# Kernel tuning notes

Measured on AMD Instinct MI355X. Metric: run time of the kernel, lower is better.

## Reference

```python
import jax, jax.numpy as jnp
import numpy as np

B, T, D = 2, 2048, 1024
H = 16
HD = D // H


def setup_inputs() -> dict:
    key = jax.random.key(0)
    ks = jax.random.split(key, 9)
    s = 1.0 / np.sqrt(D)
    return {
        "x": jax.random.normal(ks[0], (B, T, D), dtype=jnp.float32),
        "Wq": jax.random.normal(ks[1], (D, D), dtype=jnp.float32) * s,
        "bq": jax.random.normal(ks[2], (D,), dtype=jnp.float32) * s,
        "Wk": jax.random.normal(ks[3], (D, D), dtype=jnp.float32) * s,
        "bk": jax.random.normal(ks[4], (D,), dtype=jnp.float32) * s,
        "Wv": jax.random.normal(ks[5], (D, D), dtype=jnp.float32) * s,
        "bv": jax.random.normal(ks[6], (D,), dtype=jnp.float32) * s,
        "Wo": jax.random.normal(ks[7], (D, D), dtype=jnp.float32) * s,
        "bo": jax.random.normal(ks[8], (D,), dtype=jnp.float32) * s,
    }


def reference(x, Wq, bq, Wk, bk, Wv, bv, Wo, bo):
    b, t, d = x.shape
    # projections; torch Linear computes x @ W.T + b
    def proj(W, bias):
        y = jnp.einsum("btd,ed->bte", x, W) + bias
        return y.reshape(b, t, H, HD).transpose(0, 2, 1, 3)  # [B,H,T,HD]
    q = proj(Wq, bq)
    k = proj(Wk, bk)
    v = proj(Wv, bv)
    scores = jnp.einsum("bhqd,bhkd->bhqk", q, k) / np.sqrt(HD)  # [B,H,T,T]
    causal = jnp.triu(jnp.ones((t, t), dtype=bool), k=1)
    scores = jnp.where(causal[None, None], jnp.float32(-1e9), scores)
    attn = jax.nn.softmax(scores, axis=-1)
    out = jnp.einsum("bhqk,bhkd->bhqd", attn, v)  # [B,H,T,HD]
    out = out.transpose(0, 2, 1, 3).reshape(b, t, d)
    return jnp.einsum("btd,ed->bte", out, Wo) + bo
```

## Files before the change

kernel.cpp:

```cpp
#include <hip/hip_runtime.h>


#define DEV __device__ __forceinline__

typedef __attribute__((ext_vector_type(8))) __bf16 bf16x8;
typedef __attribute__((ext_vector_type(4))) float f32x4;

DEV unsigned short f2bf(float f) {
  union { float f; unsigned u; } c;
  c.f = f;
  unsigned u = c.u + 0x7FFFu + ((c.u >> 16) & 1u);
  return (unsigned short)(u >> 16);
}

DEV unsigned cvtpk(float lo, float hi) {
  unsigned r;
  asm("v_cvt_pk_bf16_f32 %0, %1, %2" : "=v"(r) : "v"(lo), "v"(hi));
  return r;
}

DEV void gload16(const unsigned short* g, unsigned short* l) {
  __builtin_amdgcn_global_load_lds(
      (const __attribute__((address_space(1))) unsigned int*)g,
      (__attribute__((address_space(3))) unsigned int*)l, 16, 0, 0);
}

DEV f32x4 mfma16(bf16x8 a, bf16x8 b, f32x4 c) {
  return __builtin_amdgcn_mfma_f32_16x16x32_bf16(a, b, c, 0, 0, 0);
}

#define WAITVM(n) asm volatile("s_waitcnt vmcnt(" #n ")" ::: "memory")
#define WAITLGKM() asm volatile("s_waitcnt lgkmcnt(0)" ::: "memory")
#define BAR() __builtin_amdgcn_s_barrier()
#define SCHEDB() __builtin_amdgcn_sched_barrier(0)

__global__ __launch_bounds__(256) void k_cvt_all(
    const float* __restrict__ x, const float* __restrict__ wq,
    const float* __restrict__ wk, const float* __restrict__ wv,
    const float* __restrict__ wo, unsigned short* __restrict__ dst) {
  int i = blockIdx.x * blockDim.x + threadIdx.x;
  const float* s;
  int off;
  if (i < 1048576) {
    s = x; off = i;
  } else {
    int j = i - 1048576;
    int w = j >> 18;
    off = j & 262143;
    s = (w == 0) ? wq : (w == 1) ? wk : (w == 2) ? wv : wo;
  }
  float4 v = reinterpret_cast<const float4*>(s)[off];
  uint2 o;
  o.x = (unsigned)f2bf(v.x) | ((unsigned)f2bf(v.y) << 16);
  o.y = (unsigned)f2bf(v.z) | ((unsigned)f2bf(v.w) << 16);
  reinterpret_cast<uint2*>(dst)[i] = o;
}

DEV void gemm_stage(const unsigned short* __restrict__ A,
                    const unsigned short* __restrict__ W,
                    unsigned short* la, unsigned short* lb,
                    int m0, int n0, int k0, int tid) {
#pragma unroll
  for (int i = 0; i < 2; ++i) {
    const int c = i * 256 + tid;
    const int row = c >> 2;
    const int scb = (((c & 3) << 4)) ^ ((row & 3) << 4);
    gload16(A + (m0 + row) * 1024 + k0 + (scb >> 1),
            (unsigned short*)((char*)la + c * 16));
    gload16(W + (n0 + row) * 1024 + k0 + (scb >> 1),
            (unsigned short*)((char*)lb + c * 16));
  }
}

DEV void gemm_core_128(const unsigned short* __restrict__ A,
                       const unsigned short* __restrict__ W,
                       unsigned short* la0, unsigned short* lb0,
                       int m0, int n0, f32x4 (&acc)[4][4]) {
  const int tid = threadIdx.x;
  const int lane = tid & 63;
  const int wave = tid >> 6;
  const int wm = (wave >> 1) * 64, wn = (wave & 1) * 64;
  const int g16 = ((lane >> 4) << 4);
  const int sx = (lane & 3) << 4;

  gemm_stage(A, W, la0, lb0, m0, n0, 0, tid);
  __syncthreads();

  for (int kt = 0; kt < 32; ++kt) {
    const int cur = kt & 1;
    unsigned short* la = la0 + cur * 4096;
    unsigned short* lb = lb0 + cur * 4096;
    if (kt + 1 < 32)
      gemm_stage(A, W, la0 + (cur ^ 1) * 4096, lb0 + (cur ^ 1) * 4096, m0, n0,
                 (kt + 1) * 32, tid);
    bf16x8 af[4], bfr[4];
#pragma unroll
    for (int m = 0; m < 4; ++m)
      af[m] = *reinterpret_cast<const bf16x8*>(
          (char*)la + (wm + m * 16 + (lane & 15)) * 64 + (g16 ^ sx));
#pragma unroll
    for (int n = 0; n < 4; ++n)
      bfr[n] = *reinterpret_cast<const bf16x8*>(
          (char*)lb + (wn + n * 16 + (lane & 15)) * 64 + (g16 ^ sx));
#pragma unroll
    for (int m = 0; m < 4; ++m)
#pragma unroll
      for (int n = 0; n < 4; ++n)
        acc[m][n] = mfma16(af[m], bfr[n], acc[m][n]);
    __syncthreads();
  }
}

__global__ __launch_bounds__(256) void k_gemm_qkv(
    const unsigned short* __restrict__ X, const unsigned short* __restrict__ Wq,
    const unsigned short* __restrict__ Wk, const unsigned short* __restrict__ Wv,
    const float* __restrict__ bq, const float* __restrict__ bk,
    const float* __restrict__ bv, unsigned short* __restrict__ Qo,
    unsigned short* __restrict__ Ko, unsigned short* __restrict__ Vo) {
  __shared__ unsigned short ls[16384];
  const int mode = blockIdx.z;
  const unsigned short* W = (mode == 0) ? Wq : (mode == 1) ? Wk : Wv;
  const float* bias = (mode == 0) ? bq : (mode == 1) ? bk : bv;
  const int m0 = blockIdx.y * 128, n0 = blockIdx.x * 128;
  f32x4 acc[4][4] = {};
  gemm_core_128(X, W, ls, ls + 8192, m0, n0, acc);

  const int lane = threadIdx.x & 63, wave = threadIdx.x >> 6;
  const int l15 = lane & 15, g = lane >> 4;
  const int wm = (wave >> 1) * 64, wn = (wave & 1) * 64;
  unsigned short* lw = ls + wave * 4096;

  const int h = (n0 + wn) >> 6;
  const int rbase0 = m0 + wm;
  const int b = rbase0 >> 11;
  const int tb0 = rbase0 & 2047;

  if (mode == 2) {
#pragma unroll
    for (int m = 0; m < 4; ++m)
#pragma unroll
      for (int n = 0; n < 4; ++n) {
        const float bb = bias[n0 + wn + n * 16 + l15];
        uint2 w;
        w.x = cvtpk(acc[m][n][0] + bb, acc[m][n][1] + bb);
        w.y = cvtpk(acc[m][n][2] + bb, acc[m][n][3] + bb);
        *reinterpret_cast<uint2*>(
            (char*)lw + (n * 16 + l15) * 128 +
            ((((m << 2) + g) ^ (l15 & 14)) << 3)) = w;
      }
    WAITLGKM();
    SCHEDB();
#pragma unroll
    for (int it = 0; it < 8; ++it) {
      const int hd = (lane >> 3) + it * 8;
      const int jj = ((lane & 7) << 1) ^ (hd & 14);
      uint4 v = *reinterpret_cast<const uint4*>((char*)lw + hd * 128 + jj * 8);
      *reinterpret_cast<uint4*>(
          &Vo[((((b << 4) + h) << 6) + hd) * 2048 + tb0 + ((lane & 7) << 3)]) =
          v;
    }
  } else {
    const float sc = (mode == 0) ? 0.180336880f : 1.0f;
#pragma unroll
    for (int m = 0; m < 4; ++m)
#pragma unroll
      for (int n = 0; n < 4; ++n) {
        const float bb = bias[n0 + wn + n * 16 + l15];
#pragma unroll
        for (int r = 0; r < 4; ++r)
          lw[(m * 16 + (g << 2) + r) * 64 + n * 16 + l15] =
              f2bf((acc[m][n][r] + bb) * sc);
      }
    WAITLGKM();
    SCHEDB();
    unsigned short* dst = (mode == 0) ? Qo : Ko;
#pragma unroll
    for (int it = 0; it < 8; ++it) {
      const int rr = (lane >> 3) + it * 8;
      const int ck = (lane & 7) * 8;
      uint4 v = *reinterpret_cast<const uint4*>(&lw[rr * 64 + ck]);
      *reinterpret_cast<uint4*>(
          &dst[(((b << 4) + h) * 2048 + tb0 + rr) * 64 + ck]) = v;
    }
  }
}

__global__ __launch_bounds__(256) void k_gemm_out(
    const unsigned short* __restrict__ Ctx, const unsigned short* __restrict__ Wo,
    const float* __restrict__ bo, float* __restrict__ Out) {
  __shared__ unsigned short ls[16384];
  unsigned short* la0 = ls;
  unsigned short* lb0 = ls + 8192;
  const int tid = threadIdx.x;
  const int lane = tid & 63, wave = tid >> 6;
  const int l15 = lane & 15, g = lane >> 4;
  const int m0 = blockIdx.y * 128, n0 = blockIdx.x * 64;
  const int wm = (wave >> 1) * 64, wn = (wave & 1) * 32;
  const int g16 = (g << 4);
  const int sx = (lane & 3) << 4;
  f32x4 acc[4][2] = {};

#define STG_OUT(buf, k0)                                                     \
  {                                                                          \
    _Pragma("unroll") for (int i = 0; i < 2; ++i) {                          \
      const int c = i * 256 + tid;                                           \
      const int row = c >> 2;                                                \
      const int scb = (((c & 3) << 4)) ^ ((row & 3) << 4);                   \
      gload16(Ctx + (m0 + row) * 1024 + (k0) + (scb >> 1),                   \
              (unsigned short*)((char*)(la0 + (buf)*4096) + c * 16));        \
    }                                                                        \
    {                                                                        \
      const int row = tid >> 2;                                              \
      const int scb = (((tid & 3) << 4)) ^ ((row & 3) << 4);                 \
      gload16(Wo + (n0 + row) * 1024 + (k0) + (scb >> 1),                    \
              (unsigned short*)((char*)(lb0 + (buf)*2048) + tid * 16));      \
    }                                                                        \
  }

  STG_OUT(0, 0);
  __syncthreads();

  for (int kt = 0; kt < 32; ++kt) {
    const int cur = kt & 1;
    unsigned short* la = la0 + cur * 4096;
    unsigned short* lb = lb0 + cur * 2048;
    if (kt + 1 < 32) STG_OUT(cur ^ 1, (kt + 1) * 32);
    bf16x8 af[4], bfr[2];
#pragma unroll
    for (int m = 0; m < 4; ++m)
      af[m] = *reinterpret_cast<const bf16x8*>(
          (char*)la + (wm + m * 16 + l15) * 64 + (g16 ^ sx));
#pragma unroll
    for (int n = 0; n < 2; ++n)
      bfr[n] = *reinterpret_cast<const bf16x8*>(
          (char*)lb + (wn + n * 16 + l15) * 64 + (g16 ^ sx));
#pragma unroll
    for (int m = 0; m < 4; ++m)
#pragma unroll
      for (int n = 0; n < 2; ++n)
        acc[m][n] = mfma16(af[m], bfr[n], acc[m][n]);
    __syncthreads();
  }
#undef STG_OUT

  float* lwf = (float*)(ls + wave * 4096);
#pragma unroll
  for (int m = 0; m < 4; ++m)
#pragma unroll
    for (int n = 0; n < 2; ++n) {
      const float bb = bo[n0 + wn + n * 16 + l15];
#pragma unroll
      for (int r = 0; r < 4; ++r)
        lwf[(m * 16 + (g << 2) + r) * 32 + n * 16 + l15] = acc[m][n][r] + bb;
    }
  WAITLGKM();
  SCHEDB();
#pragma unroll
  for (int it = 0; it < 8; ++it) {
    const int rr = (lane >> 3) + it * 8;
    const int ck = (lane & 7) * 4;
    float4 v = *reinterpret_cast<const float4*>(&lwf[rr * 32 + ck]);
    *reinterpret_cast<float4*>(&Out[(m0 + wm + rr) * 1024 + n0 + wn + ck]) = v;
  }
}


DEV void attn_stage(const unsigned short* __restrict__ Kb,
                    const unsigned short* __restrict__ Vb,
                    unsigned short* lk, unsigned short* lv, int kv0, int tid) {
#pragma unroll
  for (int i = 0; i < 2; ++i) {
    const int c = i * 256 + tid;
    const int row = c >> 3;
    const int cb = (c & 7) << 4;
    const int scb = cb ^ ((row & 7) << 4);
    gload16(Kb + (kv0 + row) * 64 + (scb >> 1),
            (unsigned short*)((char*)lk + c * 16));
    gload16(Vb + row * 2048 + kv0 + (scb >> 1),
            (unsigned short*)((char*)lv + c * 16));
  }
}

DEV void attn_step(const unsigned short* lk, const unsigned short* lv,
                   unsigned short (&lp)[16][72], const bf16x8 (&qf)[2],
                   f32x4 (&o)[4], float& lsum, int lane, int qloc, bool diag) {
  const int g = lane >> 4;
  f32x4 st[4];
#pragma unroll
  for (int n = 0; n < 4; ++n) {
    f32x4 z = {};
    const int row = n * 16 + (lane & 15);
    const int sw = (row & 7) << 4;
#pragma unroll
    for (int kk = 0; kk < 2; ++kk) {
      bf16x8 kf = *reinterpret_cast<const bf16x8*>(
          (char*)lk + row * 128 + ((kk * 64 + (g << 4)) ^ sw));
      z = mfma16(kf, qf[kk], z);
    }
    st[n] = z;
  }
  if (diag) {
#pragma unroll
    for (int n = 0; n < 4; ++n)
#pragma unroll
      for (int r = 0; r < 4; ++r)
        if (n * 16 + g * 4 + r > qloc) st[n][r] = -1e30f;
  }
  float rs = 0.f;
#pragma unroll
  for (int n = 0; n < 4; ++n)
#pragma unroll
    for (int r = 0; r < 4; ++r) {
      float p = exp2f(st[n][r]);
      st[n][r] = p;
      rs += p;
    }
  lsum += rs;
#pragma unroll
  for (int n = 0; n < 4; ++n) {
    uint2 w;
    w.x = cvtpk(st[n][0], st[n][1]);
    w.y = cvtpk(st[n][2], st[n][3]);
    *reinterpret_cast<uint2*>(&lp[lane & 15][n * 16 + g * 4]) = w;
  }
  WAITLGKM();
  SCHEDB();
  bf16x8 pb[2];
  pb[0] = *reinterpret_cast<const bf16x8*>(&lp[lane & 15][g * 8]);
  pb[1] = *reinterpret_cast<const bf16x8*>(&lp[lane & 15][32 + g * 8]);
#pragma unroll
  for (int h = 0; h < 4; ++h) {
    const int row = h * 16 + (lane & 15);
    const int sw = (row & 7) << 4;
#pragma unroll
    for (int kk = 0; kk < 2; ++kk) {
      bf16x8 vf = *reinterpret_cast<const bf16x8*>(
          (char*)lv + row * 128 + ((kk * 64 + (g << 4)) ^ sw));
      o[h] = mfma16(vf, pb[kk], o[h]);
    }
  }
}

DEV void attn_step_dual(const unsigned short* lk, const unsigned short* lv,
                        unsigned short (&lpA)[16][72],
                        unsigned short (&lpB)[16][72],
                        const bf16x8 (&qfA)[2], const bf16x8 (&qfB)[2],
                        f32x4 (&oA)[4], f32x4 (&oB)[4], float& lsA, float& lsB,
                        int lane, int qloc, bool diagA) {
  const int g = lane >> 4;
  f32x4 sA[4], sB[4];
#pragma unroll
  for (int n = 0; n < 4; ++n) {
    f32x4 zA = {}, zB = {};
    const int row = n * 16 + (lane & 15);
    const int sw = (row & 7) << 4;
#pragma unroll
    for (int kk = 0; kk < 2; ++kk) {
      bf16x8 kf = *reinterpret_cast<const bf16x8*>(
          (char*)lk + row * 128 + ((kk * 64 + (g << 4)) ^ sw));
      zB = mfma16(kf, qfB[kk], zB);
      zA = mfma16(kf, qfA[kk], zA);
    }
    sA[n] = zA;
    sB[n] = zB;
  }
  if (diagA) {
#pragma unroll
    for (int n = 0; n < 4; ++n)
#pragma unroll
      for (int r = 0; r < 4; ++r)
        if (n * 16 + g * 4 + r > qloc) sA[n][r] = -1e30f;
  }
  float rsA = 0.f, rsB = 0.f;
#pragma unroll
  for (int n = 0; n < 4; ++n)
#pragma unroll
    for (int r = 0; r < 4; ++r) {
      float pA = exp2f(sA[n][r]);
      float pB = exp2f(sB[n][r]);
      sA[n][r] = pA;
      sB[n][r] = pB;
      rsA += pA;
      rsB += pB;
    }
  lsA += rsA;
  lsB += rsB;
#pragma unroll
  for (int n = 0; n < 4; ++n) {
    uint2 wA, wB;
    wA.x = cvtpk(sA[n][0], sA[n][1]);
    wA.y = cvtpk(sA[n][2], sA[n][3]);
    wB.x = cvtpk(sB[n][0], sB[n][1]);
    wB.y = cvtpk(sB[n][2], sB[n][3]);
    *reinterpret_cast<uint2*>(&lpA[lane & 15][n * 16 + g * 4]) = wA;
    *reinterpret_cast<uint2*>(&lpB[lane & 15][n * 16 + g * 4]) = wB;
  }
  WAITLGKM();
  SCHEDB();
  bf16x8 pbA[2], pbB[2];
  pbA[0] = *reinterpret_cast<const bf16x8*>(&lpA[lane & 15][g * 8]);
  pbA[1] = *reinterpret_cast<const bf16x8*>(&lpA[lane & 15][32 + g * 8]);
  pbB[0] = *reinterpret_cast<const bf16x8*>(&lpB[lane & 15][g * 8]);
  pbB[1] = *reinterpret_cast<const bf16x8*>(&lpB[lane & 15][32 + g * 8]);
#pragma unroll
  for (int h = 0; h < 4; ++h) {
    const int row = h * 16 + (lane & 15);
    const int sw = (row & 7) << 4;
#pragma unroll
    for (int kk = 0; kk < 2; ++kk) {
      bf16x8 vf = *reinterpret_cast<const bf16x8*>(
          (char*)lv + row * 128 + ((kk * 64 + (g << 4)) ^ sw));
      oB[h] = mfma16(vf, pbB[kk], oB[h]);
      oA[h] = mfma16(vf, pbA[kk], oA[h]);
    }
  }
}

DEV void attn_epi(unsigned short* __restrict__ Ctx,
                  unsigned short (&lp)[16][72], const f32x4 (&o)[4],
                  float lsum, int b, int hh, int qbase, int lane) {
  float lt = lsum;
  lt += __shfl_xor(lt, 16);
  lt += __shfl_xor(lt, 32);
  const float inv = 1.f / lt;
  const int g = lane >> 4;
#pragma unroll
  for (int h = 0; h < 4; ++h) {
    uint2 w;
    w.x = cvtpk(o[h][0] * inv, o[h][1] * inv);
    w.y = cvtpk(o[h][2] * inv, o[h][3] * inv);
    *reinterpret_cast<uint2*>(&lp[lane & 15][h * 16 + g * 4]) = w;
  }
  WAITLGKM();
  SCHEDB();
#pragma unroll
  for (int it = 0; it < 2; ++it) {
    const int q = (lane >> 3) + it * 8;
    const int ck = (lane & 7) * 8;
    uint4 v = *reinterpret_cast<const uint4*>(&lp[q][ck]);
    *reinterpret_cast<uint4*>(
        &Ctx[(b * 2048 + qbase + q) * 1024 + hh * 64 + ck]) = v;
  }
}

__global__ __launch_bounds__(256) void k_attn(
    const unsigned short* __restrict__ Q, const unsigned short* __restrict__ K,
    const unsigned short* __restrict__ Vt, unsigned short* __restrict__ Ctx) {
  __shared__ unsigned short lk[3][64 * 64];
  __shared__ unsigned short lv[3][64 * 64];
  __shared__ unsigned short lp[8][16][72];

  const int tid = threadIdx.x, lane = tid & 63, wave = tid >> 6;
  const int ip = blockIdx.x, bh = blockIdx.y;
  const int qtA = ip;
  const int qtB = 31 - ip;
  const int nt = qtB + 1;

  const unsigned short* Kb = K + bh * 2048 * 64;
  const unsigned short* Vb = Vt + bh * 64 * 2048;

  bf16x8 qfA[2], qfB[2];
  {
    const unsigned short* qr =
        Q + (bh * 2048 + qtA * 64 + wave * 16 + (lane & 15)) * 64 + ((lane >> 4) << 3);
    qfA[0] = *reinterpret_cast<const bf16x8*>(qr);
    qfA[1] = *reinterpret_cast<const bf16x8*>(qr + 32);
    qr = Q + (bh * 2048 + qtB * 64 + wave * 16 + (lane & 15)) * 64 + ((lane >> 4) << 3);
    qfB[0] = *reinterpret_cast<const bf16x8*>(qr);
    qfB[1] = *reinterpret_cast<const bf16x8*>(qr + 32);
  }

  f32x4 oA[4] = {}, oB[4] = {};
  float lA = 0.f, lB = 0.f;
  const int qloc = wave * 16 + (lane & 15);

  attn_stage(Kb, Vb, lk[0], lv[0], 0, tid);
  attn_stage(Kb, Vb, lk[1], lv[1], 64, tid);
  WAITVM(4);
  BAR();

  for (int t = 0; t < nt; ++t) {
    const int nx = (t + 2 < nt) ? t + 2 : nt - 1;
    const int sb = (t + 2) % 3, cb = t % 3;
    attn_stage(Kb, Vb, lk[sb], lv[sb], nx * 64, tid);
    WAITVM(8);
    BAR();
    SCHEDB();
    if (t <= qtA)
      attn_step_dual(lk[cb], lv[cb], lp[wave], lp[wave + 4], qfA, qfB, oA,
                     oB, lA, lB, lane, qloc, t == qtA);
    else
      attn_step(lk[cb], lv[cb], lp[wave + 4], qfB, oB, lB, lane, qloc,
                t == qtB);
    BAR();
  }

  const int b = bh >> 4, hh = bh & 15;
  attn_epi(Ctx, lp[wave], oA, lA, b, hh, qtA * 64 + wave * 16, lane);
  attn_epi(Ctx, lp[wave + 4], oB, lB, b, hh, qtB * 64 + wave * 16, lane);
}

extern "C" void kernel_launch(void* const* d_in, const int* in_sizes, int n_in,
                              void* d_out, int out_size, void* d_ws,
                              size_t ws_size, hipStream_t stream) {
  const float* x = (const float*)d_in[0];
  const float* Wq = (const float*)d_in[1];
  const float* bq = (const float*)d_in[2];
  const float* Wk = (const float*)d_in[3];
  const float* bk = (const float*)d_in[4];
  const float* Wv = (const float*)d_in[5];
  const float* bv = (const float*)d_in[6];
  const float* Wo = (const float*)d_in[7];
  const float* bo = (const float*)d_in[8];
  float* out = (float*)d_out;

  char* ws = (char*)d_ws;
  unsigned short* xb = (unsigned short*)(ws);
  unsigned short* wqb = (unsigned short*)(ws + (8u << 20));
  unsigned short* wkb = (unsigned short*)(ws + (10u << 20));
  unsigned short* wvb = (unsigned short*)(ws + (12u << 20));
  unsigned short* wob = (unsigned short*)(ws + (14u << 20));
  unsigned short* Qb = (unsigned short*)(ws + (16u << 20));
  unsigned short* Kb = (unsigned short*)(ws + (24u << 20));
  unsigned short* Vtb = (unsigned short*)(ws + (32u << 20));
  unsigned short* Ctx = (unsigned short*)(ws + (40u << 20));

  k_cvt_all<<<8192, 256, 0, stream>>>(x, Wq, Wk, Wv, Wo, xb);

  k_gemm_qkv<<<dim3(8, 32, 3), 256, 0, stream>>>(xb, wqb, wkb, wvb, bq, bk, bv,
                                                 Qb, Kb, Vtb);
  k_attn<<<dim3(16, 32), 256, 0, stream>>>(Qb, Kb, Vtb, Ctx);
  k_gemm_out<<<dim3(16, 32), 256, 0, stream>>>(Ctx, wob, bo, out);
}
```

Measured before the change: 124.6 us.

## Software-pipeline attention loop: overlap QK of tile t with softmax/PV of t-1

Splits the per-tile attention step into a QK score phase and a softmax plus PV phase. The loop now computes the scores for tile t while finishing the exponentials and PV products for tile t-1, so MFMA work and dependent ALU work from neighbouring tiles can interleave. The V staging ring grows from 3 to 4 buffers so the previous tile's V stays valid. The loop also drops from two barriers per iteration to one. In exchange it holds more registers for the carried score tiles and uses more LDS, which may reduce occupancy.

```diff
diff --git a/kernel.cpp b/kernel.cpp
--- a/kernel.cpp
+++ b/kernel.cpp
@@ -281,11 +281,9 @@
   }
 }
 
-DEV void attn_step(const unsigned short* lk, const unsigned short* lv,
-                   unsigned short (&lp)[16][72], const bf16x8 (&qf)[2],
-                   f32x4 (&o)[4], float& lsum, int lane, int qloc, bool diag) {
+DEV void qk1(const unsigned short* lk, const bf16x8 (&qf)[2], f32x4 (&st)[4],
+             int lane, int qloc, bool diag) {
   const int g = lane >> 4;
-  f32x4 st[4];
 #pragma unroll
   for (int n = 0; n < 4; ++n) {
     f32x4 z = {};
@@ -306,21 +304,54 @@
       for (int r = 0; r < 4; ++r)
         if (n * 16 + g * 4 + r > qloc) st[n][r] = -1e30f;
   }
+}
+
+DEV void qk_dual(const unsigned short* lk, const bf16x8 (&qfA)[2],
+                 const bf16x8 (&qfB)[2], f32x4 (&sA)[4], f32x4 (&sB)[4],
+                 int lane, int qloc, bool diagA) {
+  const int g = lane >> 4;
+#pragma unroll
+  for (int n = 0; n < 4; ++n) {
+    f32x4 zA = {}, zB = {};
+    const int row = n * 16 + (lane & 15);
+    const int sw = (row & 7) << 4;
+#pragma unroll
+    for (int kk = 0; kk < 2; ++kk) {
+      bf16x8 kf = *reinterpret_cast<const bf16x8*>(
+          (char*)lk + row * 128 + ((kk * 64 + (g << 4)) ^ sw));
+      zB = mfma16(kf, qfB[kk], zB);
+      zA = mfma16(kf, qfA[kk], zA);
+    }
+    sA[n] = zA;
+    sB[n] = zB;
+  }
+  if (diagA) {
+#pragma unroll
+    for (int n = 0; n < 4; ++n)
+#pragma unroll
+      for (int r = 0; r < 4; ++r)
+        if (n * 16 + g * 4 + r > qloc) sA[n][r] = -1e30f;
+  }
+}
+
+DEV void finish1(const unsigned short* lv, unsigned short (&lp)[16][72],
+                 f32x4 (&p)[4], f32x4 (&o)[4], float& lsum, int lane) {
+  const int g = lane >> 4;
   float rs = 0.f;
 #pragma unroll
   for (int n = 0; n < 4; ++n)
 #pragma unroll
     for (int r = 0; r < 4; ++r) {
-      float p = exp2f(st[n][r]);
-      st[n][r] = p;
-      rs += p;
+      float v = exp2f(p[n][r]);
+      p[n][r] = v;
+      rs += v;
     }
   lsum += rs;
 #pragma unroll
   for (int n = 0; n < 4; ++n) {
     uint2 w;
-    w.x = cvtpk(st[n][0], st[n][1]);
-    w.y = cvtpk(st[n][2], st[n][3]);
+    w.x = cvtpk(p[n][0], p[n][1]);
+    w.y = cvtpk(p[n][2], p[n][3]);
     *reinterpret_cast<uint2*>(&lp[lane & 15][n * 16 + g * 4]) = w;
   }
   WAITLGKM();
@@ -341,57 +372,32 @@
   }
 }
 
-DEV void attn_step_dual(const unsigned short* lk, const unsigned short* lv,
-                        unsigned short (&lpA)[16][72],
-                        unsigned short (&lpB)[16][72],
-                        const bf16x8 (&qfA)[2], const bf16x8 (&qfB)[2],
-                        f32x4 (&oA)[4], f32x4 (&oB)[4], float& lsA, float& lsB,
-                        int lane, int qloc, bool diagA) {
+DEV void finish_dual(const unsigned short* lv, unsigned short (&lpA)[16][72],
+                     unsigned short (&lpB)[16][72], f32x4 (&pA)[4],
+                     f32x4 (&pB)[4], f32x4 (&oA)[4], f32x4 (&oB)[4],
+                     float& lsA, float& lsB, int lane) {
   const int g = lane >> 4;
-  f32x4 sA[4], sB[4];
-#pragma unroll
-  for (int n = 0; n < 4; ++n) {
-    f32x4 zA = {}, zB = {};
-    const int row = n * 16 + (lane & 15);
-    const int sw = (row & 7) << 4;
-#pragma unroll
-    for (int kk = 0; kk < 2; ++kk) {
-      bf16x8 kf = *reinterpret_cast<const bf16x8*>(
-          (char*)lk + row * 128 + ((kk * 64 + (g << 4)) ^ sw));
-      zB = mfma16(kf, qfB[kk], zB);
-      zA = mfma16(kf, qfA[kk], zA);
-    }
-    sA[n] = zA;
-    sB[n] = zB;
-  }
-  if (diagA) {
-#pragma unroll
-    for (int n = 0; n < 4; ++n)
-#pragma unroll
-      for (int r = 0; r < 4; ++r)
-        if (n * 16 + g * 4 + r > qloc) sA[n][r] = -1e30f;
-  }
   float rsA = 0.f, rsB = 0.f;
 #pragma unroll
   for (int n = 0; n < 4; ++n)
 #pragma unroll
     for (int r = 0; r < 4; ++r) {
-      float pA = exp2f(sA[n][r]);
-      float pB = exp2f(sB[n][r]);
-      sA[n][r] = pA;
-      sB[n][r] = pB;
-      rsA += pA;
-      rsB += pB;
+      float vA = exp2f(pA[n][r]);
+      float vB = exp2f(pB[n][r]);
+      pA[n][r] = vA;
+      pB[n][r] = vB;
+      rsA += vA;
+      rsB += vB;
     }
   lsA += rsA;
   lsB += rsB;
 #pragma unroll
   for (int n = 0; n < 4; ++n) {
     uint2 wA, wB;
-    wA.x = cvtpk(sA[n][0], sA[n][1]);
-    wA.y = cvtpk(sA[n][2], sA[n][3]);
-    wB.x = cvtpk(sB[n][0], sB[n][1]);
-    wB.y = cvtpk(sB[n][2], sB[n][3]);
+    wA.x = cvtpk(pA[n][0], pA[n][1]);
+    wA.y = cvtpk(pA[n][2], pA[n][3]);
+    wB.x = cvtpk(pB[n][0], pB[n][1]);
+    wB.y = cvtpk(pB[n][2], pB[n][3]);
     *reinterpret_cast<uint2*>(&lpA[lane & 15][n * 16 + g * 4]) = wA;
     *reinterpret_cast<uint2*>(&lpB[lane & 15][n * 16 + g * 4]) = wB;
   }
@@ -446,8 +452,8 @@
 __global__ __launch_bounds__(256) void k_attn(
     const unsigned short* __restrict__ Q, const unsigned short* __restrict__ K,
     const unsigned short* __restrict__ Vt, unsigned short* __restrict__ Ctx) {
-  __shared__ unsigned short lk[3][64 * 64];
-  __shared__ unsigned short lv[3][64 * 64];
+  __shared__ unsigned short lk[3 * 4096];
+  __shared__ unsigned short lv[4 * 4096];
   __shared__ unsigned short lp[8][16][72];
 
   const int tid = threadIdx.x, lane = tid & 63, wave = tid >> 6;
@@ -471,29 +477,43 @@
   }
 
   f32x4 oA[4] = {}, oB[4] = {};
+  f32x4 pA[4], pB[4];
   float lA = 0.f, lB = 0.f;
   const int qloc = wave * 16 + (lane & 15);
 
-  attn_stage(Kb, Vb, lk[0], lv[0], 0, tid);
-  attn_stage(Kb, Vb, lk[1], lv[1], 64, tid);
-  WAITVM(4);
-  BAR();
+  attn_stage(Kb, Vb, lk, lv, 0, tid);
+  attn_stage(Kb, Vb, lk + 4096, lv + 4096, 64, tid);
 
   for (int t = 0; t < nt; ++t) {
-    const int nx = (t + 2 < nt) ? t + 2 : nt - 1;
-    const int sb = (t + 2) % 3, cb = t % 3;
-    attn_stage(Kb, Vb, lk[sb], lv[sb], nx * 64, tid);
-    WAITVM(8);
+    WAITVM(4);
     BAR();
-    SCHEDB();
-    if (t <= qtA)
-      attn_step_dual(lk[cb], lv[cb], lp[wave], lp[wave + 4], qfA, qfB, oA,
-                     oB, lA, lB, lane, qloc, t == qtA);
+    {
+      const int nx = (t + 2 < nt) ? t + 2 : nt - 1;
+      attn_stage(Kb, Vb, lk + ((t + 2) % 3) * 4096, lv + ((t + 2) & 3) * 4096,
+                 nx * 64, tid);
+    }
+    const unsigned short* lkc = lk + (t % 3) * 4096;
+    f32x4 sA[4], sB[4];
+    const bool dual = (t <= qtA);
+    if (dual)
+      qk_dual(lkc, qfA, qfB, sA, sB, lane, qloc, t == qtA);
     else
-      attn_step(lk[cb], lv[cb], lp[wave + 4], qfB, oB, lB, lane, qloc,
-                t == qtB);
-    BAR();
-  }
+      qk1(lkc, qfB, sB, lane, qloc, t == qtB);
+    if (t > 0) {
+      const unsigned short* lvp = lv + ((t - 1) & 3) * 4096;
+      if (t - 1 <= qtA)
+        finish_dual(lvp, lp[wave], lp[wave + 4], pA, pB, oA, oB, lA, lB, lane);
+      else
+        finish1(lvp, lp[wave + 4], pB, oB, lB, lane);
+    }
+#pragma unroll
+    for (int n = 0; n < 4; ++n) pB[n] = sB[n];
+    if (dual) {
+#pragma unroll
+      for (int n = 0; n < 4; ++n) pA[n] = sA[n];
+    }
+  }
+  finish1(lv + ((nt - 1) & 3) * 4096, lp[wave + 4], pB, oB, lB, lane);
 
   const int b = bh >> 4, hh = bh & 15;
   attn_epi(Ctx, lp[wave], oA, lA, b, hh, qtA * 64 + wave * 16, lane);
```

New measurement: 171.3 us. 37.5% more time.

## Split paired causal query tiles across 8 waves and add MFMA priority hints

Applied to the files above, without the earlier changes.

The attention kernel moves from 256 to 512 threads per block. Waves 0-3 process the late query tile B and waves 4-7 the early tile A, replacing the dual-tile step in which each wave handled both. Each thread now stages one 16-byte chunk of K and V per tile, and the vmcnt waits are adjusted to match. s_setprio raises wave priority around the MFMA sections. The goal is more wave-level parallelism and latency hiding with fewer registers per wave, but the A waves go idle at the barriers for the remainder of the loop.

```diff
diff --git a/kernel.cpp b/kernel.cpp
--- a/kernel.cpp
+++ b/kernel.cpp
@@ -33,6 +33,7 @@
 #define WAITLGKM() asm volatile("s_waitcnt lgkmcnt(0)" ::: "memory")
 #define BAR() __builtin_amdgcn_s_barrier()
 #define SCHEDB() __builtin_amdgcn_sched_barrier(0)
+#define PRIO(n) __builtin_amdgcn_s_setprio(n)
 
 __global__ __launch_bounds__(256) void k_cvt_all(
     const float* __restrict__ x, const float* __restrict__ wq,
@@ -268,17 +269,14 @@
 DEV void attn_stage(const unsigned short* __restrict__ Kb,
                     const unsigned short* __restrict__ Vb,
                     unsigned short* lk, unsigned short* lv, int kv0, int tid) {
-#pragma unroll
-  for (int i = 0; i < 2; ++i) {
-    const int c = i * 256 + tid;
-    const int row = c >> 3;
-    const int cb = (c & 7) << 4;
-    const int scb = cb ^ ((row & 7) << 4);
-    gload16(Kb + (kv0 + row) * 64 + (scb >> 1),
-            (unsigned short*)((char*)lk + c * 16));
-    gload16(Vb + row * 2048 + kv0 + (scb >> 1),
-            (unsigned short*)((char*)lv + c * 16));
-  }
+  const int c = tid;
+  const int row = c >> 3;
+  const int cb = (c & 7) << 4;
+  const int scb = cb ^ ((row & 7) << 4);
+  gload16(Kb + (kv0 + row) * 64 + (scb >> 1),
+          (unsigned short*)((char*)lk + c * 16));
+  gload16(Vb + row * 2048 + kv0 + (scb >> 1),
+          (unsigned short*)((char*)lv + c * 16));
 }
 
 DEV void attn_step(const unsigned short* lk, const unsigned short* lv,
@@ -286,6 +284,7 @@
                    f32x4 (&o)[4], float& lsum, int lane, int qloc, bool diag) {
   const int g = lane >> 4;
   f32x4 st[4];
+  PRIO(1);
 #pragma unroll
   for (int n = 0; n < 4; ++n) {
     f32x4 z = {};
@@ -299,6 +298,7 @@
     }
     st[n] = z;
   }
+  PRIO(0);
   if (diag) {
 #pragma unroll
     for (int n = 0; n < 4; ++n)
@@ -328,6 +328,7 @@
   bf16x8 pb[2];
   pb[0] = *reinterpret_cast<const bf16x8*>(&lp[lane & 15][g * 8]);
   pb[1] = *reinterpret_cast<const bf16x8*>(&lp[lane & 15][32 + g * 8]);
+  PRIO(1);
 #pragma unroll
   for (int h = 0; h < 4; ++h) {
     const int row = h * 16 + (lane & 15);
@@ -339,81 +340,7 @@
       o[h] = mfma16(vf, pb[kk], o[h]);
     }
   }
-}
-
-DEV void attn_step_dual(const unsigned short* lk, const unsigned short* lv,
-                        unsigned short (&lpA)[16][72],
-                        unsigned short (&lpB)[16][72],
-                        const bf16x8 (&qfA)[2], const bf16x8 (&qfB)[2],
-                        f32x4 (&oA)[4], f32x4 (&oB)[4], float& lsA, float& lsB,
-                        int lane, int qloc, bool diagA) {
-  const int g = lane >> 4;
-  f32x4 sA[4], sB[4];
-#pragma unroll
-  for (int n = 0; n < 4; ++n) {
-    f32x4 zA = {}, zB = {};
-    const int row = n * 16 + (lane & 15);
-    const int sw = (row & 7) << 4;
-#pragma unroll
-    for (int kk = 0; kk < 2; ++kk) {
-      bf16x8 kf = *reinterpret_cast<const bf16x8*>(
-          (char*)lk + row * 128 + ((kk * 64 + (g << 4)) ^ sw));
-      zB = mfma16(kf, qfB[kk], zB);
-      zA = mfma16(kf, qfA[kk], zA);
-    }
-    sA[n] = zA;
-    sB[n] = zB;
-  }
-  if (diagA) {
-#pragma unroll
-    for (int n = 0; n < 4; ++n)
-#pragma unroll
-      for (int r = 0; r < 4; ++r)
-        if (n * 16 + g * 4 + r > qloc) sA[n][r] = -1e30f;
-  }
-  float rsA = 0.f, rsB = 0.f;
-#pragma unroll
-  for (int n = 0; n < 4; ++n)
-#pragma unroll
-    for (int r = 0; r < 4; ++r) {
-      float pA = exp2f(sA[n][r]);
-      float pB = exp2f(sB[n][r]);
-      sA[n][r] = pA;
-      sB[n][r] = pB;
-      rsA += pA;
-      rsB += pB;
-    }
-  lsA += rsA;
-  lsB += rsB;
-#pragma unroll
-  for (int n = 0; n < 4; ++n) {
-    uint2 wA, wB;
-    wA.x = cvtpk(sA[n][0], sA[n][1]);
-    wA.y = cvtpk(sA[n][2], sA[n][3]);
-    wB.x = cvtpk(sB[n][0], sB[n][1]);
-    wB.y = cvtpk(sB[n][2], sB[n][3]);
-    *reinterpret_cast<uint2*>(&lpA[lane & 15][n * 16 + g * 4]) = wA;
-    *reinterpret_cast<uint2*>(&lpB[lane & 15][n * 16 + g * 4]) = wB;
-  }
-  WAITLGKM();
-  SCHEDB();
-  bf16x8 pbA[2], pbB[2];
-  pbA[0] = *reinterpret_cast<const bf16x8*>(&lpA[lane & 15][g * 8]);
-  pbA[1] = *reinterpret_cast<const bf16x8*>(&lpA[lane & 15][32 + g * 8]);
-  pbB[0] = *reinterpret_cast<const bf16x8*>(&lpB[lane & 15][g * 8]);
-  pbB[1] = *reinterpret_cast<const bf16x8*>(&lpB[lane & 15][32 + g * 8]);
-#pragma unroll
-  for (int h = 0; h < 4; ++h) {
-    const int row = h * 16 + (lane & 15);
-    const int sw = (row & 7) << 4;
-#pragma unroll
-    for (int kk = 0; kk < 2; ++kk) {
-      bf16x8 vf = *reinterpret_cast<const bf16x8*>(
-          (char*)lv + row * 128 + ((kk * 64 + (g << 4)) ^ sw));
-      oB[h] = mfma16(vf, pbB[kk], oB[h]);
-      oA[h] = mfma16(vf, pbA[kk], oA[h]);
-    }
-  }
+  PRIO(0);
 }
 
 DEV void attn_epi(unsigned short* __restrict__ Ctx,
@@ -443,11 +370,11 @@
   }
 }
 
-__global__ __launch_bounds__(256) void k_attn(
+__global__ __launch_bounds__(512) void k_attn(
     const unsigned short* __restrict__ Q, const unsigned short* __restrict__ K,
     const unsigned short* __restrict__ Vt, unsigned short* __restrict__ Ctx) {
-  __shared__ unsigned short lk[3][64 * 64];
-  __shared__ unsigned short lv[3][64 * 64];
+  __shared__ unsigned short lk[3 * 4096];
+  __shared__ unsigned short lv[3 * 4096];
   __shared__ unsigned short lp[8][16][72];
 
   const int tid = threadIdx.x, lane = tid & 63, wave = tid >> 6;
@@ -456,48 +383,47 @@
   const int qtB = 31 - ip;
   const int nt = qtB + 1;
 
+  const bool isB = wave < 4;
+  const int wv4 = wave & 3;
+  const int qt = isB ? qtB : qtA;
+  const int myNt = isB ? nt : qtA + 1;
+
   const unsigned short* Kb = K + bh * 2048 * 64;
   const unsigned short* Vb = Vt + bh * 64 * 2048;
 
-  bf16x8 qfA[2], qfB[2];
+  bf16x8 qf[2];
   {
     const unsigned short* qr =
-        Q + (bh * 2048 + qtA * 64 + wave * 16 + (lane & 15)) * 64 + ((lane >> 4) << 3);
-    qfA[0] = *reinterpret_cast<const bf16x8*>(qr);
-    qfA[1] = *reinterpret_cast<const bf16x8*>(qr + 32);
-    qr = Q + (bh * 2048 + qtB * 64 + wave * 16 + (lane & 15)) * 64 + ((lane >> 4) << 3);
-    qfB[0] = *reinterpret_cast<const bf16x8*>(qr);
-    qfB[1] = *reinterpret_cast<const bf16x8*>(qr + 32);
-  }
-
-  f32x4 oA[4] = {}, oB[4] = {};
-  float lA = 0.f, lB = 0.f;
-  const int qloc = wave * 16 + (lane & 15);
-
-  attn_stage(Kb, Vb, lk[0], lv[0], 0, tid);
-  attn_stage(Kb, Vb, lk[1], lv[1], 64, tid);
-  WAITVM(4);
+        Q + (bh * 2048 + qt * 64 + wv4 * 16 + (lane & 15)) * 64 +
+        ((lane >> 4) << 3);
+    qf[0] = *reinterpret_cast<const bf16x8*>(qr);
+    qf[1] = *reinterpret_cast<const bf16x8*>(qr + 32);
+  }
+
+  f32x4 o[4] = {};
+  float lsum = 0.f;
+  const int qloc = wv4 * 16 + (lane & 15);
+
+  attn_stage(Kb, Vb, lk, lv, 0, tid);
+  attn_stage(Kb, Vb, lk + 4096, lv + 4096, 64, tid);
+  WAITVM(2);
   BAR();
 
   for (int t = 0; t < nt; ++t) {
     const int nx = (t + 2 < nt) ? t + 2 : nt - 1;
-    const int sb = (t + 2) % 3, cb = t % 3;
-    attn_stage(Kb, Vb, lk[sb], lv[sb], nx * 64, tid);
-    WAITVM(8);
+    attn_stage(Kb, Vb, lk + ((t + 2) % 3) * 4096, lv + ((t + 2) % 3) * 4096,
+               nx * 64, tid);
+    WAITVM(4);
     BAR();
     SCHEDB();
-    if (t <= qtA)
-      attn_step_dual(lk[cb], lv[cb], lp[wave], lp[wave + 4], qfA, qfB, oA,
-                     oB, lA, lB, lane, qloc, t == qtA);
-    else
-      attn_step(lk[cb], lv[cb], lp[wave + 4], qfB, oB, lB, lane, qloc,
-                t == qtB);
+    if (t < myNt)
+      attn_step(lk + (t % 3) * 4096, lv + (t % 3) * 4096, lp[wave], qf, o,
+                lsum, lane, qloc, t == qt);
     BAR();
   }
 
   const int b = bh >> 4, hh = bh & 15;
-  attn_epi(Ctx, lp[wave], oA, lA, b, hh, qtA * 64 + wave * 16, lane);
-  attn_epi(Ctx, lp[wave + 4], oB, lB, b, hh, qtB * 64 + wave * 16, lane);
+  attn_epi(Ctx, lp[wave], o, lsum, b, hh, qt * 64 + wv4 * 16, lane);
 }
 
 extern "C" void kernel_launch(void* const* d_in, const int* in_sizes, int n_in,
@@ -529,6 +455,6 @@
 
   k_gemm_qkv<<<dim3(8, 32, 3), 256, 0, stream>>>(xb, wqb, wkb, wvb, bq, bk, bv,
                                                  Qb, Kb, Vtb);
-  k_attn<<<dim3(16, 32), 256, 0, stream>>>(Qb, Kb, Vtb, Ctx);
+  k_attn<<<dim3(16, 32), 512, 0, stream>>>(Qb, Kb, Vtb, Ctx);
   k_gemm_out<<<dim3(16, 32), 256, 0, stream>>>(Ctx, wob, bo, out);
 }
```

Result: faster. 120.9 us (-3.0%).
